# Performance work log

Measured on AMD Instinct MI355X. Metric: run time of the kernel, lower is better.

Reference implementation:

```python
import jax, jax.numpy as jnp
import numpy as np

N_CLASS, EMB, NH = 32000, 128, 256
B, T = 2048, 256


def setup_inputs() -> dict:
    key = jax.random.key(0)
    ks = iter(jax.random.split(key, 40))
    d = {}
    d["X"] = jax.random.randint(next(ks), (B, T), 0, N_CLASS)
    d["C"] = jax.random.normal(next(ks), (N_CLASS, EMB), jnp.float32) * 0.02
    for g in "ifco":
        d[f"U_{g}1"] = jax.random.normal(next(ks), (EMB, NH), jnp.float32) / np.sqrt(EMB)
        d[f"V_{g}1"] = jax.random.normal(next(ks), (NH, NH), jnp.float32) / np.sqrt(NH)
        d[f"U_{g}2"] = jax.random.normal(next(ks), (NH, NH), jnp.float32) / np.sqrt(NH)
        d[f"V_{g}2"] = jax.random.normal(next(ks), (NH, NH), jnp.float32) / np.sqrt(NH)
        d[f"b_{g}1"] = jnp.ones((NH,), jnp.float32)
    d["W_out"] = jax.random.normal(next(ks), (NH, N_CLASS), jnp.float32) / np.sqrt(NH)
    d["b_out"] = jnp.ones((N_CLASS,), jnp.float32)
    return d


def reference(X, C,
              U_i1, V_i1, U_i2, V_i2, b_i1,
              U_f1, V_f1, U_f2, V_f2, b_f1,
              U_c1, V_c1, U_c2, V_c2, b_c1,
              U_o1, V_o1, U_o2, V_o2, b_o1,
              W_out, b_out):
    # Embed then move time to the leading axis: [T, B, EMB]
    xs = jnp.transpose(C[X], (1, 0, 2))
    Bsz = X.shape[0]
    dtype = C.dtype
    z = jnp.zeros((Bsz, NH), dtype)

    def step(carry, x):
        h1, c1, h2, c2 = carry
        # layer 1 LSTM cell
        f1 = jax.nn.sigmoid(x @ U_f1 + h1 @ V_f1 + b_f1)
        i1 = jax.nn.sigmoid(x @ U_i1 + h1 @ V_i1 + b_i1)
        g1 = jnp.tanh(x @ U_c1 + h1 @ V_c1 + b_c1)
        c1n = c1 * f1 + i1 * g1
        o1 = jax.nn.sigmoid(x @ U_o1 + h1 @ V_o1 + b_o1)
        h1n = o1 * jnp.tanh(c1n)
        # layer 2 LSTM cell (NOTE: original code reuses layer-1 biases here)
        f2 = jax.nn.sigmoid(h1n @ U_f2 + h2 @ V_f2 + b_f1)
        i2 = jax.nn.sigmoid(h1n @ U_i2 + h2 @ V_i2 + b_i1)
        g2 = jnp.tanh(h1n @ U_c2 + h2 @ V_c2 + b_c1)
        c2n = c2 * f2 + i2 * g2
        o2 = jax.nn.sigmoid(h1n @ U_o2 + h2 @ V_o2 + b_o1)
        h2n = o2 * jnp.tanh(c2n)
        return (h1n, c1n, h2n, c2n), None

    (h1, c1, h2, c2), _ = jax.lax.scan(step, (z, z, z, z), xs)
    return h2 @ W_out + b_out  # [B, N_CLASS]
```

## Files before the change

kernel.cpp:

```cpp
#include <hip/hip_runtime.h>
#include <hip/hip_bf16.h>

#define B_SZ   2048
#define T_SZ   256
#define EMB    128
#define NH     256
#define NCLASS 32000

typedef __bf16 bf16;
typedef __bf16 bf16x8 __attribute__((ext_vector_type(8)));
typedef float  f32x4  __attribute__((ext_vector_type(4)));

__device__ __forceinline__ float sigf(float x)      { return 1.0f / (1.0f + __expf(-x)); }
__device__ __forceinline__ float tanhfast(float x)  { return 2.0f / (1.0f + __expf(-2.0f * x)) - 1.0f; }

struct GatePtrs {
    const float* U1[4];
    const float* V1[4];
    const float* U2[4];
    const float* V2[4];
};

__global__ void prep_w1(GatePtrs gp, bf16* __restrict__ Wt1) {
    int gc = blockIdx.x;
    int k  = threadIdx.x;
    int g  = (gc >> 4) & 3;
    int nh = ((gc >> 6) << 4) | (gc & 15);
    float v = (k < EMB) ? gp.U1[g][k * NH + nh] : gp.V1[g][(k - EMB) * NH + nh];
    Wt1[gc * 384 + k] = (bf16)v;
}

__global__ void prep_w2(GatePtrs gp, bf16* __restrict__ Wt2) {
    int gc = blockIdx.x;
    int k  = threadIdx.x;
    int g  = (gc >> 4) & 3;
    int nh = ((gc >> 6) << 4) | (gc & 15);
    float v = (k < NH) ? gp.U2[g][k * NH + nh] : gp.V2[g][(k - NH) * NH + nh];
    Wt2[gc * 512 + k] = (bf16)v;
}

__global__ void prep_wo(const float* __restrict__ Wo, bf16* __restrict__ WoT) {
    __shared__ float tile[32][33];
    int n0 = blockIdx.x * 32;
    int k0 = blockIdx.y * 32;
    int tx = threadIdx.x & 31;
    int ty = threadIdx.x >> 5;
#pragma unroll
    for (int i = 0; i < 4; i++) {
        int k = k0 + ty + i * 8;
        tile[ty + i * 8][tx] = Wo[(size_t)k * NCLASS + n0 + tx];
    }
    __syncthreads();
#pragma unroll
    for (int i = 0; i < 4; i++) {
        int n = n0 + ty + i * 8;
        WoT[(size_t)n * NH + k0 + tx] = (bf16)tile[tx][ty + i * 8];
    }
}

__global__ __launch_bounds__(512, 1) void lstm_kernel(
    const int* __restrict__ X, const float* __restrict__ C,
    const bf16* __restrict__ Wt1, const bf16* __restrict__ Wt2,
    const float* __restrict__ bi, const float* __restrict__ bf_,
    const float* __restrict__ bc, const float* __restrict__ bo,
    bf16* __restrict__ h2out)
{
    __shared__ bf16 A1[32][392];
    __shared__ bf16 A2[32][520];

    const int tid  = threadIdx.x;
    const int lane = tid & 63;
    const int wv   = tid >> 6;
    const int cl   = lane & 15;
    const int quad = lane >> 4;
    const int gb   = blockIdx.x * 32;

    const float* bp[4] = { bi, bf_, bc, bo };
    float bias[2][4];
#pragma unroll
    for (int hg = 0; hg < 2; hg++)
#pragma unroll
        for (int g = 0; g < 4; g++)
            bias[hg][g] = bp[g][wv * 32 + hg * 16 + cl];

    for (int i = tid; i < 8192; i += 512) {
        int r = i >> 8, c = i & 255;
        A1[r][128 + c] = (bf16)0.0f;
        A2[r][256 + c] = (bf16)0.0f;
    }
    {
        int r  = tid >> 4;
        int cc = (tid & 15) * 8;
        int idx = X[(gb + r) * T_SZ + 0];
        const float* src = C + (size_t)idx * EMB + cc;
        float4 v0 = *(const float4*)(src);
        float4 v1 = *(const float4*)(src + 4);
        bf16x8 hv;
        hv[0] = (bf16)v0.x; hv[1] = (bf16)v0.y; hv[2] = (bf16)v0.z; hv[3] = (bf16)v0.w;
        hv[4] = (bf16)v1.x; hv[5] = (bf16)v1.y; hv[6] = (bf16)v1.z; hv[7] = (bf16)v1.w;
        *(bf16x8*)&A1[r][cc] = hv;
    }

    f32x4 c1s[2][2], c2s[2][2];
    const f32x4 zf = { 0.0f, 0.0f, 0.0f, 0.0f };
#pragma unroll
    for (int a = 0; a < 2; a++)
#pragma unroll
        for (int b = 0; b < 2; b++) { c1s[a][b] = zf; c2s[a][b] = zf; }

    __syncthreads();

    for (int t = 0; t < T_SZ; t++) {
        f32x4 acc[2][2][4];
#pragma unroll
        for (int mt = 0; mt < 2; mt++)
#pragma unroll
            for (int hg = 0; hg < 2; hg++)
#pragma unroll
                for (int g = 0; g < 4; g++) acc[mt][hg][g] = zf;

#pragma unroll
        for (int kt = 0; kt < 12; kt++) {
            bf16x8 a0 = *(const bf16x8*)&A1[cl][kt * 32 + quad * 8];
            bf16x8 a1 = *(const bf16x8*)&A1[16 + cl][kt * 32 + quad * 8];
#pragma unroll
            for (int hg = 0; hg < 2; hg++)
#pragma unroll
                for (int g = 0; g < 4; g++) {
                    int gc = (wv * 2 + hg) * 64 + g * 16 + cl;
                    bf16x8 b = *(const bf16x8*)(Wt1 + gc * 384 + kt * 32 + quad * 8);
                    acc[0][hg][g] = __builtin_amdgcn_mfma_f32_16x16x32_bf16(a0, b, acc[0][hg][g], 0, 0, 0);
                    acc[1][hg][g] = __builtin_amdgcn_mfma_f32_16x16x32_bf16(a1, b, acc[1][hg][g], 0, 0, 0);
                }
        }
        __syncthreads();

#pragma unroll
        for (int mt = 0; mt < 2; mt++)
#pragma unroll
            for (int hg = 0; hg < 2; hg++)
#pragma unroll
                for (int r = 0; r < 4; r++) {
                    float iv = sigf(acc[mt][hg][0][r] + bias[hg][0]);
                    float fv = sigf(acc[mt][hg][1][r] + bias[hg][1]);
                    float gv = tanhfast(acc[mt][hg][2][r] + bias[hg][2]);
                    float ov = sigf(acc[mt][hg][3][r] + bias[hg][3]);
                    float c  = c1s[mt][hg][r] * fv + iv * gv;
                    c1s[mt][hg][r] = c;
                    float h  = ov * tanhfast(c);
                    int row = mt * 16 + quad * 4 + r;
                    int col = wv * 32 + hg * 16 + cl;
                    bf16 hb = (bf16)h;
                    A1[row][128 + col] = hb;
                    A2[row][col]       = hb;
                }

        if (t + 1 < T_SZ) {
            int r  = tid >> 4;
            int cc = (tid & 15) * 8;
            int idx = X[(gb + r) * T_SZ + (t + 1)];
            const float* src = C + (size_t)idx * EMB + cc;
            float4 v0 = *(const float4*)(src);
            float4 v1 = *(const float4*)(src + 4);
            bf16x8 hv;
            hv[0] = (bf16)v0.x; hv[1] = (bf16)v0.y; hv[2] = (bf16)v0.z; hv[3] = (bf16)v0.w;
            hv[4] = (bf16)v1.x; hv[5] = (bf16)v1.y; hv[6] = (bf16)v1.z; hv[7] = (bf16)v1.w;
            *(bf16x8*)&A1[r][cc] = hv;
        }
        __syncthreads();

#pragma unroll
        for (int mt = 0; mt < 2; mt++)
#pragma unroll
            for (int hg = 0; hg < 2; hg++)
#pragma unroll
                for (int g = 0; g < 4; g++) acc[mt][hg][g] = zf;

#pragma unroll
        for (int kt = 0; kt < 16; kt++) {
            bf16x8 a0 = *(const bf16x8*)&A2[cl][kt * 32 + quad * 8];
            bf16x8 a1 = *(const bf16x8*)&A2[16 + cl][kt * 32 + quad * 8];
#pragma unroll
            for (int hg = 0; hg < 2; hg++)
#pragma unroll
                for (int g = 0; g < 4; g++) {
                    int gc = (wv * 2 + hg) * 64 + g * 16 + cl;
                    bf16x8 b = *(const bf16x8*)(Wt2 + gc * 512 + kt * 32 + quad * 8);
                    acc[0][hg][g] = __builtin_amdgcn_mfma_f32_16x16x32_bf16(a0, b, acc[0][hg][g], 0, 0, 0);
                    acc[1][hg][g] = __builtin_amdgcn_mfma_f32_16x16x32_bf16(a1, b, acc[1][hg][g], 0, 0, 0);
                }
        }
        __syncthreads();

#pragma unroll
        for (int mt = 0; mt < 2; mt++)
#pragma unroll
            for (int hg = 0; hg < 2; hg++)
#pragma unroll
                for (int r = 0; r < 4; r++) {
                    float iv = sigf(acc[mt][hg][0][r] + bias[hg][0]);
                    float fv = sigf(acc[mt][hg][1][r] + bias[hg][1]);
                    float gv = tanhfast(acc[mt][hg][2][r] + bias[hg][2]);
                    float ov = sigf(acc[mt][hg][3][r] + bias[hg][3]);
                    float c  = c2s[mt][hg][r] * fv + iv * gv;
                    c2s[mt][hg][r] = c;
                    float h  = ov * tanhfast(c);
                    int row = mt * 16 + quad * 4 + r;
                    int col = wv * 32 + hg * 16 + cl;
                    A2[row][256 + col] = (bf16)h;
                }
    }

    __syncthreads();
    for (int i = tid; i < 8192; i += 512) {
        int r = i >> 8, c = i & 255;
        h2out[(size_t)(gb + r) * NH + c] = A2[r][256 + c];
    }
}

__global__ __launch_bounds__(256, 1) void out_gemm(
    const bf16* __restrict__ h2, const bf16* __restrict__ WoT,
    const float* __restrict__ bout, float* __restrict__ out)
{
    const int tid  = threadIdx.x;
    const int lane = tid & 63;
    const int wv   = tid >> 6;
    const int cl   = lane & 15;
    const int quad = lane >> 4;
    const int nb   = blockIdx.x;
    const int mb   = blockIdx.y;
    const int mbase = mb * 64 + wv * 16;
    const int nbase = nb * 64;

    f32x4 acc[4];
    const f32x4 zf = { 0.0f, 0.0f, 0.0f, 0.0f };
#pragma unroll
    for (int nt = 0; nt < 4; nt++) acc[nt] = zf;

#pragma unroll
    for (int kt = 0; kt < 8; kt++) {
        bf16x8 a = *(const bf16x8*)(h2 + (size_t)(mbase + cl) * NH + kt * 32 + quad * 8);
#pragma unroll
        for (int nt = 0; nt < 4; nt++) {
            bf16x8 b = *(const bf16x8*)(WoT + (size_t)(nbase + nt * 16 + cl) * NH + kt * 32 + quad * 8);
            acc[nt] = __builtin_amdgcn_mfma_f32_16x16x32_bf16(a, b, acc[nt], 0, 0, 0);
        }
    }
#pragma unroll
    for (int nt = 0; nt < 4; nt++) {
        int col = nbase + nt * 16 + cl;
        float bv = bout[col];
#pragma unroll
        for (int r = 0; r < 4; r++) {
            int row = mbase + quad * 4 + r;
            out[(size_t)row * NCLASS + col] = acc[nt][r] + bv;
        }
    }
}

extern "C" void kernel_launch(void* const* d_in, const int* in_sizes, int n_in,
                              void* d_out, int out_size, void* d_ws, size_t ws_size,
                              hipStream_t stream) {
    const int*   X  = (const int*)d_in[0];
    const float* C  = (const float*)d_in[1];
    GatePtrs gp;
    for (int g = 0; g < 4; g++) {
        int base = 2 + 5 * g;
        gp.U1[g] = (const float*)d_in[base + 0];
        gp.V1[g] = (const float*)d_in[base + 1];
        gp.U2[g] = (const float*)d_in[base + 2];
        gp.V2[g] = (const float*)d_in[base + 3];
    }
    const float* bi   = (const float*)d_in[6];
    const float* bf_  = (const float*)d_in[11];
    const float* bc   = (const float*)d_in[16];
    const float* bo   = (const float*)d_in[21];
    const float* Wo   = (const float*)d_in[22];
    const float* bout = (const float*)d_in[23];
    float* out = (float*)d_out;

    char* ws = (char*)d_ws;
    bf16* Wt1 = (bf16*)(ws);
    bf16* Wt2 = (bf16*)(ws + 786432);
    bf16* WoT = (bf16*)(ws + 786432 + 1048576);
    bf16* h2w = (bf16*)(ws + 786432 + 1048576 + 16384000);

    prep_w1<<<dim3(1024), dim3(384), 0, stream>>>(gp, Wt1);
    prep_w2<<<dim3(1024), dim3(512), 0, stream>>>(gp, Wt2);
    prep_wo<<<dim3(1000, 8), dim3(256), 0, stream>>>(Wo, WoT);
    lstm_kernel<<<dim3(64), dim3(512), 0, stream>>>(X, C, Wt1, Wt2, bi, bf_, bc, bo, h2w);
    out_gemm<<<dim3(500, 32), dim3(256), 0, stream>>>(h2w, WoT, bout, out);
}
```

Measured before the change: 14.71 ms.

## Split LSTM across 256 cooperating blocks with global flag sync and register-resident weights

The recurrent kernel is restructured from 64 independent blocks into 256 blocks. Each group of 8 blocks shares a 64-row batch slice and splits the hidden columns among them. Hidden states are exchanged through double-buffered global buffers, with atomic per-timestep flags and spin-waits between blocks. Layer-1 and layer-2 are computed by separate wave halves, pipelined one step apart. Weights are held in registers, the MFMA moves to 32x32x16, and LDS gets an XOR swizzle. The aim is to use far more CUs on the serial recurrence, at the cost of inter-block spin synchronisation that assumes all 256 blocks are co-resident, plus a timeout guard that could silently give wrong results.

```diff
diff --git a/kernel.cpp b/kernel.cpp
--- a/kernel.cpp
+++ b/kernel.cpp
@@ -1,18 +1,26 @@
 #include <hip/hip_runtime.h>
 #include <hip/hip_bf16.h>
 
-#define B_SZ   2048
 #define T_SZ   256
 #define EMB    128
 #define NH     256
 #define NCLASS 32000
+#define BSZ    2048
+#define BH     (BSZ * NH)
 
 typedef __bf16 bf16;
 typedef __bf16 bf16x8 __attribute__((ext_vector_type(8)));
 typedef float  f32x4  __attribute__((ext_vector_type(4)));
-
-__device__ __forceinline__ float sigf(float x)      { return 1.0f / (1.0f + __expf(-x)); }
-__device__ __forceinline__ float tanhfast(float x)  { return 2.0f / (1.0f + __expf(-2.0f * x)) - 1.0f; }
+typedef float  f32x16 __attribute__((ext_vector_type(16)));
+
+#define A1S  392
+#define A2S  264
+#define GSTR 33
+
+__device__ __forceinline__ float sigf(float x)     { return 1.0f / (1.0f + __expf(-x)); }
+__device__ __forceinline__ float tanhfast(float x) { return 2.0f / (1.0f + __expf(-2.0f * x)) - 1.0f; }
+
+__device__ __forceinline__ int chsw(int row, int c) { return c ^ (((row >> 3) & 3) << 1); }
 
 struct GatePtrs {
     const float* U1[4];
@@ -24,8 +32,8 @@
 __global__ void prep_w1(GatePtrs gp, bf16* __restrict__ Wt1) {
     int gc = blockIdx.x;
     int k  = threadIdx.x;
-    int g  = (gc >> 4) & 3;
-    int nh = ((gc >> 6) << 4) | (gc & 15);
+    int g  = (gc >> 3) & 3;
+    int nh = ((gc >> 5) << 3) | (gc & 7);
     float v = (k < EMB) ? gp.U1[g][k * NH + nh] : gp.V1[g][(k - EMB) * NH + nh];
     Wt1[gc * 384 + k] = (bf16)v;
 }
@@ -33,8 +41,8 @@
 __global__ void prep_w2(GatePtrs gp, bf16* __restrict__ Wt2) {
     int gc = blockIdx.x;
     int k  = threadIdx.x;
-    int g  = (gc >> 4) & 3;
-    int nh = ((gc >> 6) << 4) | (gc & 15);
+    int g  = (gc >> 3) & 3;
+    int nh = ((gc >> 5) << 3) | (gc & 7);
     float v = (k < NH) ? gp.U2[g][k * NH + nh] : gp.V2[g][(k - NH) * NH + nh];
     Wt2[gc * 512 + k] = (bf16)v;
 }
@@ -58,163 +66,253 @@
     }
 }
 
-__global__ __launch_bounds__(512, 1) void lstm_kernel(
+__device__ __forceinline__ void flag_add(int* p) {
+    __hip_atomic_fetch_add(p, 1, __ATOMIC_RELEASE, __HIP_MEMORY_SCOPE_AGENT);
+}
+__device__ __forceinline__ bool spin8(int* p, bool dead) {
+    if (dead) return true;
+    int guard = 0;
+    while (__hip_atomic_load(p, __ATOMIC_ACQUIRE, __HIP_MEMORY_SCOPE_AGENT) < 8) {
+        __builtin_amdgcn_s_sleep(2);
+        if (++guard > (4 << 20)) return true;
+    }
+    return false;
+}
+
+__device__ __forceinline__ void zero16(f32x16& v) {
+#pragma unroll
+    for (int i = 0; i < 16; i++) v[i] = 0.0f;
+}
+
+__device__ __forceinline__ void stage_x(const int* __restrict__ X, const float* __restrict__ C,
+                                        bf16* A1, int gb, int t, int tid) {
+    if (t >= T_SZ) return;
+    int r   = tid >> 3;
+    int seg = tid & 7;
+    int idx = X[(gb + r) * T_SZ + t];
+    const float4* src = (const float4*)(C + (size_t)idx * EMB + seg * 16);
+    float4 v0 = src[0], v1 = src[1], v2 = src[2], v3 = src[3];
+    bf16x8 h0, h1v;
+    h0[0]=(bf16)v0.x; h0[1]=(bf16)v0.y; h0[2]=(bf16)v0.z; h0[3]=(bf16)v0.w;
+    h0[4]=(bf16)v1.x; h0[5]=(bf16)v1.y; h0[6]=(bf16)v1.z; h0[7]=(bf16)v1.w;
+    h1v[0]=(bf16)v2.x; h1v[1]=(bf16)v2.y; h1v[2]=(bf16)v2.z; h1v[3]=(bf16)v2.w;
+    h1v[4]=(bf16)v3.x; h1v[5]=(bf16)v3.y; h1v[6]=(bf16)v3.z; h1v[7]=(bf16)v3.w;
+    int c0 = seg * 2;
+    *(bf16x8*)(A1 + r * A1S + chsw(r, c0) * 8)     = h0;
+    *(bf16x8*)(A1 + r * A1S + chsw(r, c0 + 1) * 8) = h1v;
+}
+
+__device__ __forceinline__ void readback(bf16* A1, bf16* A2,
+                                         const bf16* __restrict__ h1p, const bf16* __restrict__ h2p,
+                                         int gb, int tid, bool do_h2) {
+#pragma unroll
+    for (int jj = 0; jj < 4; jj++) {
+        int q   = tid + 512 * jj;
+        int row = q >> 5;
+        int c   = q & 31;
+        bf16x8 v = *(const bf16x8*)(h1p + (size_t)(gb + row) * NH + c * 8);
+        *(bf16x8*)(A1 + row * A1S + chsw(row, 16 + c) * 8) = v;
+        if (do_h2) {
+            bf16x8 u = *(const bf16x8*)(h2p + (size_t)(gb + row) * NH + c * 8);
+            *(bf16x8*)(A2 + row * A2S + chsw(row, c) * 8) = u;
+        }
+    }
+}
+
+__device__ __forceinline__ void acc_to_G(float* Gw, const f32x16& a0, const f32x16& a1, int lane) {
+    int col = lane & 31;
+    int rh  = 4 * (lane >> 5);
+#pragma unroll
+    for (int r = 0; r < 16; r++) {
+        int row0 = (r & 3) + 8 * (r >> 2) + rh;
+        Gw[row0 * GSTR + col]        = a0[r];
+        Gw[(row0 + 32) * GSTR + col] = a1[r];
+    }
+}
+
+__device__ __forceinline__ void ew_store(const float* Gw, const float* BI, float (&cst)[8],
+                                         bf16* __restrict__ hbuf, int gb, int lane, int nhb) {
+    bf16x8 hv;
+    const float* gr = Gw + lane * GSTR;
+#pragma unroll
+    for (int j = 0; j < 8; j++) {
+        int nh = nhb * 8 + j;
+        float pi = gr[0 + j]  + BI[0 * 256 + nh];
+        float pf = gr[8 + j]  + BI[1 * 256 + nh];
+        float pg = gr[16 + j] + BI[2 * 256 + nh];
+        float po = gr[24 + j] + BI[3 * 256 + nh];
+        float iv = sigf(pi), fv = sigf(pf), gv = tanhfast(pg), ov = sigf(po);
+        float cc = cst[j] * fv + iv * gv;
+        cst[j] = cc;
+        hv[j] = (bf16)(ov * tanhfast(cc));
+    }
+    *(bf16x8*)(hbuf + (size_t)(gb + lane) * NH + nhb * 8) = hv;
+}
+
+__global__ __launch_bounds__(512, 2) void lstm_kernel(
     const int* __restrict__ X, const float* __restrict__ C,
     const bf16* __restrict__ Wt1, const bf16* __restrict__ Wt2,
-    const float* __restrict__ bi, const float* __restrict__ bf_,
-    const float* __restrict__ bc, const float* __restrict__ bo,
-    bf16* __restrict__ h2out)
+    const float* __restrict__ b0, const float* __restrict__ b1,
+    const float* __restrict__ b2, const float* __restrict__ b3,
+    bf16* __restrict__ h1buf, bf16* __restrict__ h2buf,
+    int* __restrict__ flags1, int* __restrict__ flags2)
 {
-    __shared__ bf16 A1[32][392];
-    __shared__ bf16 A2[32][520];
+    extern __shared__ char smem_raw[];
+    bf16*  A1 = (bf16*)smem_raw;
+    bf16*  A2 = (bf16*)(smem_raw + 50176);
+    float* G  = (float*)(smem_raw + 50176 + 33792);
+    float* BI = (float*)(smem_raw + 50176 + 33792 + 67584);
 
     const int tid  = threadIdx.x;
     const int lane = tid & 63;
     const int wv   = tid >> 6;
-    const int cl   = lane & 15;
-    const int quad = lane >> 4;
-    const int gb   = blockIdx.x * 32;
-
-    const float* bp[4] = { bi, bf_, bc, bo };
-    float bias[2][4];
-#pragma unroll
-    for (int hg = 0; hg < 2; hg++)
-#pragma unroll
-        for (int g = 0; g < 4; g++)
-            bias[hg][g] = bp[g][wv * 32 + hg * 16 + cl];
-
-    for (int i = tid; i < 8192; i += 512) {
-        int r = i >> 8, c = i & 255;
-        A1[r][128 + c] = (bf16)0.0f;
-        A2[r][256 + c] = (bf16)0.0f;
-    }
+    const int blk  = blockIdx.x;
+    const int xcd  = blk & 7;
+    const int j5   = blk >> 3;
+    const int bg   = xcd * 4 + (j5 & 3);
+    const int cg   = j5 >> 2;
+    const int gb   = bg * 64;
+    int* f1 = flags1 + bg * 512;
+    int* f2 = flags2 + bg * 512;
+
     {
-        int r  = tid >> 4;
-        int cc = (tid & 15) * 8;
-        int idx = X[(gb + r) * T_SZ + 0];
-        const float* src = C + (size_t)idx * EMB + cc;
-        float4 v0 = *(const float4*)(src);
-        float4 v1 = *(const float4*)(src + 4);
-        bf16x8 hv;
-        hv[0] = (bf16)v0.x; hv[1] = (bf16)v0.y; hv[2] = (bf16)v0.z; hv[3] = (bf16)v0.w;
-        hv[4] = (bf16)v1.x; hv[5] = (bf16)v1.y; hv[6] = (bf16)v1.z; hv[7] = (bf16)v1.w;
-        *(bf16x8*)&A1[r][cc] = hv;
-    }
-
-    f32x4 c1s[2][2], c2s[2][2];
-    const f32x4 zf = { 0.0f, 0.0f, 0.0f, 0.0f };
-#pragma unroll
-    for (int a = 0; a < 2; a++)
-#pragma unroll
-        for (int b = 0; b < 2; b++) { c1s[a][b] = zf; c2s[a][b] = zf; }
-
+        const float* bp[4] = { b0, b1, b2, b3 };
+        for (int i = tid; i < 1024; i += 512) BI[i] = bp[i >> 8][i & 255];
+    }
+    {
+        bf16x8 z;
+#pragma unroll
+        for (int i = 0; i < 8; i++) z[i] = (bf16)0.0f;
+        for (int q = tid; q < 2048; q += 512) {
+            int row = q >> 5, c = q & 31;
+            *(bf16x8*)(A1 + row * A1S + chsw(row, 16 + c) * 8) = z;
+            *(bf16x8*)(A2 + row * A2S + chsw(row, c) * 8) = z;
+        }
+    }
+    stage_x(X, C, A1, gb, 0, tid);
     __syncthreads();
 
-    for (int t = 0; t < T_SZ; t++) {
-        f32x4 acc[2][2][4];
-#pragma unroll
-        for (int mt = 0; mt < 2; mt++)
-#pragma unroll
-            for (int hg = 0; hg < 2; hg++)
-#pragma unroll
-                for (int g = 0; g < 4; g++) acc[mt][hg][g] = zf;
-
-#pragma unroll
-        for (int kt = 0; kt < 12; kt++) {
-            bf16x8 a0 = *(const bf16x8*)&A1[cl][kt * 32 + quad * 8];
-            bf16x8 a1 = *(const bf16x8*)&A1[16 + cl][kt * 32 + quad * 8];
-#pragma unroll
-            for (int hg = 0; hg < 2; hg++)
-#pragma unroll
-                for (int g = 0; g < 4; g++) {
-                    int gc = (wv * 2 + hg) * 64 + g * 16 + cl;
-                    bf16x8 b = *(const bf16x8*)(Wt1 + gc * 384 + kt * 32 + quad * 8);
-                    acc[0][hg][g] = __builtin_amdgcn_mfma_f32_16x16x32_bf16(a0, b, acc[0][hg][g], 0, 0, 0);
-                    acc[1][hg][g] = __builtin_amdgcn_mfma_f32_16x16x32_bf16(a1, b, acc[1][hg][g], 0, 0, 0);
+    const int hk   = lane >> 5;
+    const int r0   = lane & 31;
+    const int swz  = ((r0 >> 3) & 3) << 1;
+    bf16* a1p0 = A1 + r0 * A1S;
+    bf16* a1p1 = A1 + (32 + r0) * A1S;
+    bf16* a2p0 = A2 + r0 * A2S;
+    bf16* a2p1 = A2 + (32 + r0) * A2S;
+    float* Gw  = G + wv * (64 * GSTR);
+    bool dead = false;
+
+    if (wv < 4) {
+        const int nhb = cg * 4 + wv;
+        bf16x8 w1[24];
+        {
+            const bf16* wp = Wt1 + (size_t)(nhb * 32 + r0) * 384 + hk * 8;
+#pragma unroll
+            for (int kt = 0; kt < 24; kt++) w1[kt] = *(const bf16x8*)(wp + kt * 16);
+        }
+        float cst[8];
+#pragma unroll
+        for (int j = 0; j < 8; j++) cst[j] = 0.0f;
+
+        {
+            f32x16 ac0, ac1; zero16(ac0); zero16(ac1);
+#pragma unroll
+            for (int kt = 0; kt < 24; kt++) {
+                int off = ((kt * 2 + hk) ^ swz) * 8;
+                bf16x8 fa0 = *(const bf16x8*)(a1p0 + off);
+                bf16x8 fa1 = *(const bf16x8*)(a1p1 + off);
+                ac0 = __builtin_amdgcn_mfma_f32_32x32x16_bf16(fa0, w1[kt], ac0, 0, 0, 0);
+                ac1 = __builtin_amdgcn_mfma_f32_32x32x16_bf16(fa1, w1[kt], ac1, 0, 0, 0);
+            }
+            acc_to_G(Gw, ac0, ac1, lane);
+            ew_store(Gw, BI, cst, h1buf , gb, lane, nhb);
+        }
+        __threadfence();
+        __syncthreads();
+        if (tid == 0) flag_add(f1 + 0);
+        dead = spin8(f1 + 0, dead);
+        readback(A1, A2, h1buf, h2buf, gb, tid, false);
+        stage_x(X, C, A1, gb, 1, tid);
+        __syncthreads();
+
+#pragma unroll 1
+        for (int t = 0; t < 256; t++) {
+            if (t < 255) {
+                f32x16 ac0, ac1; zero16(ac0); zero16(ac1);
+#pragma unroll
+                for (int kt = 0; kt < 24; kt++) {
+                    int off = ((kt * 2 + hk) ^ swz) * 8;
+                    bf16x8 fa0 = *(const bf16x8*)(a1p0 + off);
+                    bf16x8 fa1 = *(const bf16x8*)(a1p1 + off);
+                    ac0 = __builtin_amdgcn_mfma_f32_32x32x16_bf16(fa0, w1[kt], ac0, 0, 0, 0);
+                    ac1 = __builtin_amdgcn_mfma_f32_32x32x16_bf16(fa1, w1[kt], ac1, 0, 0, 0);
                 }
-        }
+                acc_to_G(Gw, ac0, ac1, lane);
+                ew_store(Gw, BI, cst, h1buf + ((t + 1) & 1) * BH, gb, lane, nhb);
+            }
+            __threadfence();
+            __syncthreads();
+            if (tid == 0 && t < 255) flag_add(f1 + t + 1);
+            if (t < 255) {
+                dead = spin8(f1 + t + 1, dead);
+                dead = spin8(f2 + t, dead);
+                readback(A1, A2, h1buf + ((t + 1) & 1) * BH, h2buf + (t & 1) * BH, gb, tid, true);
+                stage_x(X, C, A1, gb, t + 2, tid);
+            }
+            __syncthreads();
+        }
+    } else {
+        const int nhb = cg * 4 + (wv - 4);
+        bf16x8 w2[32];
+        {
+            const bf16* wp = Wt2 + (size_t)(nhb * 32 + r0) * 512 + hk * 8;
+#pragma unroll
+            for (int kt = 0; kt < 32; kt++) w2[kt] = *(const bf16x8*)(wp + kt * 16);
+        }
+        float cst[8];
+#pragma unroll
+        for (int j = 0; j < 8; j++) cst[j] = 0.0f;
+
         __syncthreads();
-
-#pragma unroll
-        for (int mt = 0; mt < 2; mt++)
-#pragma unroll
-            for (int hg = 0; hg < 2; hg++)
-#pragma unroll
-                for (int r = 0; r < 4; r++) {
-                    float iv = sigf(acc[mt][hg][0][r] + bias[hg][0]);
-                    float fv = sigf(acc[mt][hg][1][r] + bias[hg][1]);
-                    float gv = tanhfast(acc[mt][hg][2][r] + bias[hg][2]);
-                    float ov = sigf(acc[mt][hg][3][r] + bias[hg][3]);
-                    float c  = c1s[mt][hg][r] * fv + iv * gv;
-                    c1s[mt][hg][r] = c;
-                    float h  = ov * tanhfast(c);
-                    int row = mt * 16 + quad * 4 + r;
-                    int col = wv * 32 + hg * 16 + cl;
-                    bf16 hb = (bf16)h;
-                    A1[row][128 + col] = hb;
-                    A2[row][col]       = hb;
+        dead = spin8(f1 + 0, dead);
+        readback(A1, A2, h1buf, h2buf, gb, tid, false);
+        stage_x(X, C, A1, gb, 1, tid);
+        __syncthreads();
+
+#pragma unroll 1
+        for (int t = 0; t < 256; t++) {
+            {
+                f32x16 ac0, ac1; zero16(ac0); zero16(ac1);
+#pragma unroll
+                for (int kt = 0; kt < 16; kt++) {
+                    int off = ((16 + kt * 2 + hk) ^ swz) * 8;
+                    bf16x8 fa0 = *(const bf16x8*)(a1p0 + off);
+                    bf16x8 fa1 = *(const bf16x8*)(a1p1 + off);
+                    ac0 = __builtin_amdgcn_mfma_f32_32x32x16_bf16(fa0, w2[kt], ac0, 0, 0, 0);
+                    ac1 = __builtin_amdgcn_mfma_f32_32x32x16_bf16(fa1, w2[kt], ac1, 0, 0, 0);
                 }
-
-        if (t + 1 < T_SZ) {
-            int r  = tid >> 4;
-            int cc = (tid & 15) * 8;
-            int idx = X[(gb + r) * T_SZ + (t + 1)];
-            const float* src = C + (size_t)idx * EMB + cc;
-            float4 v0 = *(const float4*)(src);
-            float4 v1 = *(const float4*)(src + 4);
-            bf16x8 hv;
-            hv[0] = (bf16)v0.x; hv[1] = (bf16)v0.y; hv[2] = (bf16)v0.z; hv[3] = (bf16)v0.w;
-            hv[4] = (bf16)v1.x; hv[5] = (bf16)v1.y; hv[6] = (bf16)v1.z; hv[7] = (bf16)v1.w;
-            *(bf16x8*)&A1[r][cc] = hv;
-        }
-        __syncthreads();
-
-#pragma unroll
-        for (int mt = 0; mt < 2; mt++)
-#pragma unroll
-            for (int hg = 0; hg < 2; hg++)
-#pragma unroll
-                for (int g = 0; g < 4; g++) acc[mt][hg][g] = zf;
-
-#pragma unroll
-        for (int kt = 0; kt < 16; kt++) {
-            bf16x8 a0 = *(const bf16x8*)&A2[cl][kt * 32 + quad * 8];
-            bf16x8 a1 = *(const bf16x8*)&A2[16 + cl][kt * 32 + quad * 8];
-#pragma unroll
-            for (int hg = 0; hg < 2; hg++)
-#pragma unroll
-                for (int g = 0; g < 4; g++) {
-                    int gc = (wv * 2 + hg) * 64 + g * 16 + cl;
-                    bf16x8 b = *(const bf16x8*)(Wt2 + gc * 512 + kt * 32 + quad * 8);
-                    acc[0][hg][g] = __builtin_amdgcn_mfma_f32_16x16x32_bf16(a0, b, acc[0][hg][g], 0, 0, 0);
-                    acc[1][hg][g] = __builtin_amdgcn_mfma_f32_16x16x32_bf16(a1, b, acc[1][hg][g], 0, 0, 0);
+#pragma unroll
+                for (int kt = 16; kt < 32; kt++) {
+                    int off = (((kt - 16) * 2 + hk) ^ swz) * 8;
+                    bf16x8 fa0 = *(const bf16x8*)(a2p0 + off);
+                    bf16x8 fa1 = *(const bf16x8*)(a2p1 + off);
+                    ac0 = __builtin_amdgcn_mfma_f32_32x32x16_bf16(fa0, w2[kt], ac0, 0, 0, 0);
+                    ac1 = __builtin_amdgcn_mfma_f32_32x32x16_bf16(fa1, w2[kt], ac1, 0, 0, 0);
                 }
-        }
-        __syncthreads();
-
-#pragma unroll
-        for (int mt = 0; mt < 2; mt++)
-#pragma unroll
-            for (int hg = 0; hg < 2; hg++)
-#pragma unroll
-                for (int r = 0; r < 4; r++) {
-                    float iv = sigf(acc[mt][hg][0][r] + bias[hg][0]);
-                    float fv = sigf(acc[mt][hg][1][r] + bias[hg][1]);
-                    float gv = tanhfast(acc[mt][hg][2][r] + bias[hg][2]);
-                    float ov = sigf(acc[mt][hg][3][r] + bias[hg][3]);
-                    float c  = c2s[mt][hg][r] * fv + iv * gv;
-                    c2s[mt][hg][r] = c;
-                    float h  = ov * tanhfast(c);
-                    int row = mt * 16 + quad * 4 + r;
-                    int col = wv * 32 + hg * 16 + cl;
-                    A2[row][256 + col] = (bf16)h;
-                }
-    }
-
-    __syncthreads();
-    for (int i = tid; i < 8192; i += 512) {
-        int r = i >> 8, c = i & 255;
-        h2out[(size_t)(gb + r) * NH + c] = A2[r][256 + c];
+                acc_to_G(Gw, ac0, ac1, lane);
+                ew_store(Gw, BI, cst, h2buf + (t & 1) * BH, gb, lane, nhb);
+            }
+            __threadfence();
+            __syncthreads();
+            if (tid == 256 && true) flag_add(f2 + t);
+            if (t < 255) {
+                dead = spin8(f1 + t + 1, dead);
+                dead = spin8(f2 + t, dead);
+                readback(A1, A2, h1buf + ((t + 1) & 1) * BH, h2buf + (t & 1) * BH, gb, tid, true);
+                stage_x(X, C, A1, gb, t + 2, tid);
+            }
+            __syncthreads();
+        }
     }
 }
 
@@ -280,14 +378,28 @@
     float* out = (float*)d_out;
 
     char* ws = (char*)d_ws;
+    const size_t OFF_WT2 = 786432;
+    const size_t OFF_WOT = 1835008;
+    const size_t OFF_H1  = 18219008;
+    const size_t OFF_H2  = 20316160;
+    const size_t OFF_FLG = 22413312;
     bf16* Wt1 = (bf16*)(ws);
-    bf16* Wt2 = (bf16*)(ws + 786432);
-    bf16* WoT = (bf16*)(ws + 786432 + 1048576);
-    bf16* h2w = (bf16*)(ws + 786432 + 1048576 + 16384000);
-
+    bf16* Wt2 = (bf16*)(ws + OFF_WT2);
+    bf16* WoT = (bf16*)(ws + OFF_WOT);
+    bf16* h1b = (bf16*)(ws + OFF_H1);
+    bf16* h2b = (bf16*)(ws + OFF_H2);
+    int*  fl1 = (int*)(ws + OFF_FLG);
+    int*  fl2 = (int*)(ws + OFF_FLG + 65536);
+
+    hipMemsetAsync(ws + OFF_FLG, 0, 131072, stream);
     prep_w1<<<dim3(1024), dim3(384), 0, stream>>>(gp, Wt1);
     prep_w2<<<dim3(1024), dim3(512), 0, stream>>>(gp, Wt2);
     prep_wo<<<dim3(1000, 8), dim3(256), 0, stream>>>(Wo, WoT);
-    lstm_kernel<<<dim3(64), dim3(512), 0, stream>>>(X, C, Wt1, Wt2, bi, bf_, bc, bo, h2w);
-    out_gemm<<<dim3(500, 32), dim3(256), 0, stream>>>(h2w, WoT, bout, out);
-}
+
+    hipFuncSetAttribute((const void*)lstm_kernel,
+                        hipFuncAttributeMaxDynamicSharedMemorySize, 155648);
+    lstm_kernel<<<dim3(256), dim3(512), 155648, stream>>>(
+        X, C, Wt1, Wt2, bi, bf_, bc, bo, h1b, h2b, fl1, fl2);
+
+    out_gemm<<<dim3(500, 32), dim3(256), 0, stream>>>(h2b + BH, WoT, bout, out);
+}
```

After: 29.21 ms. 98.6% more time.
